# Optimization experiments

Measured on AMD Instinct MI355X. Metric: run time of the kernel, lower is better.

## Reference

```python
import jax, jax.numpy as jnp
import numpy as np

NTOKENS = 50257
NHID = 1024
NTOK_PER_CLASS = 225   # ceil(sqrt(50257))
NCLASSES = 224         # ceil(50257/225)
BATCH = 2048


def setup_inputs() -> dict:
    key = jax.random.key(0)
    k1, k2, k3, k4 = jax.random.split(key, 4)
    initrange = 0.1
    inputs = jax.random.normal(k1, (BATCH, NHID), dtype=jnp.float32)
    labels = jax.random.randint(k2, (BATCH,), 0, NTOKENS, dtype=jnp.int64)
    layer_top_W = jax.random.uniform(k3, (NHID, NCLASSES), dtype=jnp.float32,
                                     minval=-initrange, maxval=initrange)
    layer_top_b = jnp.zeros((NCLASSES,), dtype=jnp.float32)
    layer_bottom_W = jax.random.uniform(k4, (NCLASSES, NHID, NTOK_PER_CLASS),
                                        dtype=jnp.float32,
                                        minval=-initrange, maxval=initrange)
    layer_bottom_b = jnp.zeros((NCLASSES, NTOK_PER_CLASS), dtype=jnp.float32)
    return {"inputs": inputs, "labels": labels,
            "layer_top_W": layer_top_W, "layer_top_b": layer_top_b,
            "layer_bottom_W": layer_bottom_W, "layer_bottom_b": layer_bottom_b}


def reference(inputs, labels, layer_top_W, layer_top_b, layer_bottom_W, layer_bottom_b):
    batch_size = inputs.shape[0]
    label_position_top = labels // NTOK_PER_CLASS          # [B]
    label_position_bottom = labels % NTOK_PER_CLASS        # [B]

    # top-level class probabilities
    top_logits = inputs @ layer_top_W + layer_top_b        # [B, nclasses]
    top_probs = jax.nn.softmax(top_logits, axis=1)

    # per-sample gather of class weight matrices + batched matmul
    W_sel = layer_bottom_W[label_position_top]             # [B, nhid, ntok_per_class]
    b_sel = layer_bottom_b[label_position_top]             # [B, ntok_per_class]
    bottom_logits = jnp.einsum('bh,bht->bt', inputs, W_sel) + b_sel
    bottom_probs = jax.nn.softmax(bottom_logits, axis=1)

    idx = jnp.arange(batch_size)
    target_probs = top_probs[idx, label_position_top] * bottom_probs[idx, label_position_bottom]
    return target_probs
```

## Files before the change

kernel.cpp:

```cpp
#include <hip/hip_runtime.h>
#include <math.h>

#define NHID  1024
#define NCLS  224
#define NTPC  225
#define BATCH 2048

#define KSPLIT 8
#define KCH    128
#define NTILES (BATCH / 16)
#define NBOT_BLOCKS (NCLS * KSPLIT)
#define NTOP_BLOCKS (NTILES * KSPLIT)

#define YTS 224
#define YBS 228
#define YTOPK (BATCH * YTS)
#define YBOTK (BATCH * YBS)

#define CLS_OFF  0
#define POS_OFF  8192
#define LIST_OFF 16384
#define OFFS_OFF 24576
#define YTOP_OFF 32768
#define YTOP_BYTES (KSPLIT * YTOPK * 4)
#define YBOT_OFF (YTOP_OFF + YTOP_BYTES)
#define YBOT_BYTES (KSPLIT * YBOTK * 4)

typedef float f4u __attribute__((ext_vector_type(4), aligned(4)));

__global__ __launch_bounds__(256) void group_kernel(const int* __restrict__ labels,
                                                    int* __restrict__ cls,
                                                    int* __restrict__ pos,
                                                    int* __restrict__ list,
                                                    int* __restrict__ offs) {
    __shared__ int cnt[NCLS];
    __shared__ int sc[256];
    __shared__ int bex[NCLS];
    __shared__ int nz;
    const int tid = threadIdx.x;
    if (tid == 0) nz = 0;
    for (int j = tid; j < NCLS; j += 256) cnt[j] = 0;
    __syncthreads();
    int loc = 0;
    for (int k = 0; k < 4; ++k) {
        int i = tid + 256 * k;
        if (labels[2 * i + 1] != 0) loc = 1;
    }
    if (loc) atomicOr(&nz, 1);
    __syncthreads();
    const bool is64 = (nz == 0);
    int myc[8], myr[8];
#pragma unroll
    for (int k = 0; k < 8; ++k) {
        int i = tid + 256 * k;
        int l = is64 ? labels[2 * i] : labels[i];
        int c = l / NTPC;
        cls[i] = c;
        pos[i] = l - c * NTPC;
        myc[k] = c;
        myr[k] = atomicAdd(&cnt[c], 1);
    }
    __syncthreads();
    int v = (tid < NCLS) ? cnt[tid] : 0;
    sc[tid] = v;
    __syncthreads();
    for (int off = 1; off < 256; off <<= 1) {
        int u = (tid >= off) ? sc[tid - off] : 0;
        __syncthreads();
        sc[tid] += u;
        __syncthreads();
    }
    if (tid < NCLS) {
        int ex = sc[tid] - v;
        bex[tid] = ex;
        offs[tid] = ex;
    }
    if (tid == 0) offs[NCLS] = BATCH;
    __syncthreads();
#pragma unroll
    for (int k = 0; k < 8; ++k) {
        int i = tid + 256 * k;
        list[bex[myc[k]] + myr[k]] = i;
    }
}

template<int YC, int YS, bool BOT>
__device__ __forceinline__ void run_tiles(const float* __restrict__ x,
                                          const float* __restrict__ W,
                                          float* __restrict__ yk,
                                          const int* __restrict__ list,
                                          int o, int n, int hbase,
                                          float* __restrict__ xs) {
    const int tid = threadIdx.x;
    const int w = tid >> 6, l = tid & 63;
    const int cb  = 4 * l;
    const int cbc = min(cb, YC - 4);
    const int r  = tid & 127;
    const int hs = tid >> 7;
    const int rq = (r >> 1) & 3;
    const float4* xsq = (const float4*)xs;

    for (int tile = 0; tile * 16 < n; ++tile) {
        if (tile) __syncthreads();
        const float* xrow = x + hbase + r;
#pragma unroll
        for (int j = 0; j < 8; ++j) {
            const int i = hs * 8 + j;
            const int idx = tile * 16 + i;
            const int s = BOT ? list[o + min(idx, n - 1)] : (o + idx);
            xs[(r << 4) + ((((i >> 2) ^ rq) << 2) | (i & 3))] = xrow[(size_t)s * NHID];
        }
        __syncthreads();

        float4 acc[4];
#pragma unroll
        for (int i = 0; i < 4; ++i) acc[i] = make_float4(0.f, 0.f, 0.f, 0.f);

        auto compute4 = [&](int hb, int ph, const f4u (&wv)[4]) {
#pragma unroll
            for (int j = 0; j < 4; ++j) {
                const float4 xv = xsq[(hb + j) * 4 + (w ^ (ph + (j >> 1)))];
                const f4u wq = wv[j];
                acc[0].x = fmaf(xv.x, wq.x, acc[0].x);
                acc[0].y = fmaf(xv.x, wq.y, acc[0].y);
                acc[0].z = fmaf(xv.x, wq.z, acc[0].z);
                acc[0].w = fmaf(xv.x, wq.w, acc[0].w);
                acc[1].x = fmaf(xv.y, wq.x, acc[1].x);
                acc[1].y = fmaf(xv.y, wq.y, acc[1].y);
                acc[1].z = fmaf(xv.y, wq.z, acc[1].z);
                acc[1].w = fmaf(xv.y, wq.w, acc[1].w);
                acc[2].x = fmaf(xv.z, wq.x, acc[2].x);
                acc[2].y = fmaf(xv.z, wq.y, acc[2].y);
                acc[2].z = fmaf(xv.z, wq.z, acc[2].z);
                acc[2].w = fmaf(xv.z, wq.w, acc[2].w);
                acc[3].x = fmaf(xv.w, wq.x, acc[3].x);
                acc[3].y = fmaf(xv.w, wq.y, acc[3].y);
                acc[3].z = fmaf(xv.w, wq.z, acc[3].z);
                acc[3].w = fmaf(xv.w, wq.w, acc[3].w);
            }
        };

        const float* wp = W + (size_t)hbase * YC + cbc;
        f4u wva[4], wvb[4];
#pragma unroll
        for (int j = 0; j < 4; ++j)
            wva[j] = *(const f4u*)(wp + (size_t)j * YC);

#pragma unroll 1
        for (int h0 = 0; h0 < KCH; h0 += 8) {
            const float* wpb = wp + 4 * (size_t)YC;
#pragma unroll
            for (int j = 0; j < 4; ++j)
                wvb[j] = *(const f4u*)(wpb + (size_t)j * YC);
            compute4(h0, 0, wva);
            const float* wpa = wp + ((h0 + 8 < KCH) ? 8 : 0) * (size_t)YC;
#pragma unroll
            for (int j = 0; j < 4; ++j)
                wva[j] = *(const f4u*)(wpa + (size_t)j * YC);
            compute4(h0 + 4, 2, wvb);
            wp += 8 * (size_t)YC;
        }

        const int nt = min(n - tile * 16, 16);
#pragma unroll
        for (int jj = 0; jj < 4; ++jj) {
            const int it = 4 * w + jj;
            if (it < nt) {
                const int s = BOT ? list[o + tile * 16 + it] : (o + tile * 16 + it);
                float* yr = yk + (size_t)s * YS;
                if (cb + 3 < YC) {
                    *(float4*)(yr + cb) = acc[jj];
                } else if (cb < YC) {
                    yr[cb] = acc[jj].w;
                }
            }
        }
    }
}

__global__ __launch_bounds__(256, 4) void partial_kernel(const float* __restrict__ x,
                                                         const float* __restrict__ Wt,
                                                         const float* __restrict__ Wb,
                                                         const int* __restrict__ list,
                                                         const int* __restrict__ offs,
                                                         float* __restrict__ ytop,
                                                         float* __restrict__ ybot) {
    __shared__ __align__(16) float xs[KCH * 16];
    const int bi = blockIdx.x;
    if (bi < NBOT_BLOCKS) {
        const int c = bi % NCLS;
        const int k = bi / NCLS;
        const int o = offs[c];
        const int n = offs[c + 1] - o;
        run_tiles<NTPC, YBS, true>(x, Wb + (size_t)c * (NHID * NTPC),
                                   ybot + (size_t)k * YBOTK, list, o, n, k * KCH, xs);
    } else {
        const int b2 = bi - NBOT_BLOCKS;
        const int st = b2 % NTILES;
        const int k  = b2 / NTILES;
        run_tiles<NCLS, YTS, false>(x, Wt, ytop + (size_t)k * YTOPK, list,
                                    st * 16, 16, k * KCH, xs);
    }
}

__global__ __launch_bounds__(256) void finalize_kernel(const float* __restrict__ ytop,
                                                       const float* __restrict__ ybot,
                                                       const float* __restrict__ bt,
                                                       const float* __restrict__ bb,
                                                       const int* __restrict__ cls,
                                                       const int* __restrict__ pos,
                                                       float* __restrict__ out) {
    const int w = threadIdx.x >> 6, l = threadIdx.x & 63;
    const int s = blockIdx.x * 4 + w;
    const int c = cls[s], p = pos[s];

    float v[4];
#pragma unroll
    for (int g = 0; g < 4; ++g) {
        int col = l + 64 * g;
        if (col < NCLS) {
            float a = bt[col];
#pragma unroll
            for (int k = 0; k < KSPLIT; ++k)
                a += ytop[(size_t)k * YTOPK + (size_t)s * YTS + col];
            v[g] = a;
        } else {
            v[g] = -INFINITY;
        }
    }
    float mx = fmaxf(fmaxf(v[0], v[1]), fmaxf(v[2], v[3]));
#pragma unroll
    for (int off = 32; off; off >>= 1) mx = fmaxf(mx, __shfl_xor(mx, off));
    float sum = 0.f, tc = 0.f;
#pragma unroll
    for (int g = 0; g < 4; ++g) {
        int col = l + 64 * g;
        float e = (col < NCLS) ? __expf(v[g] - mx) : 0.f;
        sum += e;
        if (col == c) tc = e;
    }
#pragma unroll
    for (int off = 32; off; off >>= 1) {
        sum += __shfl_xor(sum, off);
        tc  += __shfl_xor(tc, off);
    }
    const float tp = tc / sum;

#pragma unroll
    for (int g = 0; g < 4; ++g) {
        int col = l + 64 * g;
        if (col < NTPC) {
            float a = bb[c * NTPC + col];
#pragma unroll
            for (int k = 0; k < KSPLIT; ++k)
                a += ybot[(size_t)k * YBOTK + (size_t)s * YBS + col];
            v[g] = a;
        } else {
            v[g] = -INFINITY;
        }
    }
    mx = fmaxf(fmaxf(v[0], v[1]), fmaxf(v[2], v[3]));
#pragma unroll
    for (int off = 32; off; off >>= 1) mx = fmaxf(mx, __shfl_xor(mx, off));
    float bsum = 0.f, ep = 0.f;
#pragma unroll
    for (int g = 0; g < 4; ++g) {
        int col = l + 64 * g;
        float e = (col < NTPC) ? __expf(v[g] - mx) : 0.f;
        bsum += e;
        if (col == p) ep = e;
    }
#pragma unroll
    for (int off = 32; off; off >>= 1) bsum += __shfl_xor(bsum, off);
#pragma unroll
    for (int g = 0; g < 4; ++g)
        if (l + 64 * g == p) out[s] = tp * ep / bsum;
}

extern "C" void kernel_launch(void* const* d_in, const int* in_sizes, int n_in,
                              void* d_out, int out_size, void* d_ws, size_t ws_size,
                              hipStream_t stream) {
    const float* inputs = (const float*)d_in[0];
    const int*   labels = (const int*)d_in[1];
    const float* topW   = (const float*)d_in[2];
    const float* topB   = (const float*)d_in[3];
    const float* botW   = (const float*)d_in[4];
    const float* botB   = (const float*)d_in[5];
    float* out = (float*)d_out;

    char* ws   = (char*)d_ws;
    int*   cls = (int*)(ws + CLS_OFF);
    int*   pos = (int*)(ws + POS_OFF);
    int*   lst = (int*)(ws + LIST_OFF);
    int*   off = (int*)(ws + OFFS_OFF);
    float* ytop = (float*)(ws + YTOP_OFF);
    float* ybot = (float*)(ws + YBOT_OFF);

    group_kernel<<<1, 256, 0, stream>>>(labels, cls, pos, lst, off);
    partial_kernel<<<NBOT_BLOCKS + NTOP_BLOCKS, 256, 0, stream>>>(
        inputs, topW, botW, lst, off, ytop, ybot);
    finalize_kernel<<<BATCH / 4, 256, 0, stream>>>(ytop, ybot, topB, botB, cls, pos, out);
}
```

Baseline: 333.8 us.

## Stage weight tiles into LDS via async global_load_lds with a producer wave

Weight rows are no longer read straight from global memory into registers. One dedicated wave issues asynchronous global-to-LDS DMA copies into a double-buffered LDS slot, synchronised with manual waitcnt and barriers, so weight fetches overlap compute. Each block now processes two 16-sample tiles per pass over the weights, halving weight traffic per sample. The LDS footprint grows, so occupancy drops from 4 to 3 blocks per SIMD launch bound. This adds padding and tail-fix logic for unaligned 225-wide rows, which carries a correctness risk.

```diff
diff --git a/kernel.cpp b/kernel.cpp
--- a/kernel.cpp
+++ b/kernel.cpp
@@ -16,6 +16,11 @@
 #define YBS 228
 #define YTOPK (BATCH * YTS)
 #define YBOTK (BATCH * YBS)
+
+#define RPAD 228
+#define WSLOT (16 * RPAD)
+#define XS_OFF (2 * WSLOT)
+#define LDS_FLOATS (2 * WSLOT + 2 * 2048)
 
 #define CLS_OFF  0
 #define POS_OFF  8192
@@ -26,7 +31,36 @@
 #define YBOT_OFF (YTOP_OFF + YTOP_BYTES)
 #define YBOT_BYTES (KSPLIT * YBOTK * 4)
 
-typedef float f4u __attribute__((ext_vector_type(4), aligned(4)));
+#define SBAR() __builtin_amdgcn_s_barrier()
+#define LGKM0() do { asm volatile("s_waitcnt lgkmcnt(0)" ::: "memory"); \
+                     __builtin_amdgcn_sched_barrier(0); } while (0)
+#define VM15() do { asm volatile("s_waitcnt vmcnt(15)" ::: "memory"); \
+                    __builtin_amdgcn_sched_barrier(0); } while (0)
+#define VM0()  do { asm volatile("s_waitcnt vmcnt(0)" ::: "memory"); \
+                    __builtin_amdgcn_sched_barrier(0); } while (0)
+
+__device__ __forceinline__ void dma16(const float* src, float* dst) {
+    __builtin_amdgcn_global_load_lds(
+        (const __attribute__((address_space(1))) void*)src,
+        (__attribute__((address_space(3))) void*)dst, 16, 0, 0);
+}
+
+template<int RBF>
+__device__ __forceinline__ void issue_group(const float* chunk, const float* wend,
+                                            float* wslot, int g, int l) {
+    const float* gb = chunk + (size_t)g * 16 * RBF;
+#pragma unroll
+    for (int i = 0; i < 15; ++i) {
+        if (i < 14 || l < 16) {
+            const int c = 64 * i + l;
+            const int row = c / 57;
+            const int b = c - row * 57;
+            const float* src = gb + row * RBF + b * 4;
+            if (src + 4 > wend) src = wend - 4;
+            dma16(src, wslot + i * 256);
+        }
+    }
+}
 
 __global__ __launch_bounds__(256) void group_kernel(const int* __restrict__ labels,
                                                     int* __restrict__ cls,
@@ -84,122 +118,143 @@
     }
 }
 
-template<int YC, int YS, bool BOT>
+template<int YC, int YS, int RBF, bool BOT>
 __device__ __forceinline__ void run_tiles(const float* __restrict__ x,
-                                          const float* __restrict__ W,
+                                          const float* __restrict__ chunk,
+                                          const float* __restrict__ wend,
                                           float* __restrict__ yk,
                                           const int* __restrict__ list,
                                           int o, int n, int hbase,
-                                          float* __restrict__ xs) {
+                                          float* __restrict__ lds) {
+    float* wlds = lds;
+    float* xsb  = lds + XS_OFF;
     const int tid = threadIdx.x;
     const int w = tid >> 6, l = tid & 63;
-    const int cb  = 4 * l;
-    const int cbc = min(cb, YC - 4);
+    const bool pw = (w == 3);
     const int r  = tid & 127;
     const int hs = tid >> 7;
     const int rq = (r >> 1) & 3;
-    const float4* xsq = (const float4*)xs;
-
-    for (int tile = 0; tile * 16 < n; ++tile) {
-        if (tile) __syncthreads();
-        const float* xrow = x + hbase + r;
-#pragma unroll
-        for (int j = 0; j < 8; ++j) {
-            const int i = hs * 8 + j;
-            const int idx = tile * 16 + i;
-            const int s = BOT ? list[o + min(idx, n - 1)] : (o + idx);
-            xs[(r << 4) + ((((i >> 2) ^ rq) << 2) | (i & 3))] = xrow[(size_t)s * NHID];
-        }
-        __syncthreads();
-
-        float4 acc[4];
-#pragma unroll
-        for (int i = 0; i < 4; ++i) acc[i] = make_float4(0.f, 0.f, 0.f, 0.f);
-
-        auto compute4 = [&](int hb, int ph, const f4u (&wv)[4]) {
-#pragma unroll
-            for (int j = 0; j < 4; ++j) {
-                const float4 xv = xsq[(hb + j) * 4 + (w ^ (ph + (j >> 1)))];
-                const f4u wq = wv[j];
-                acc[0].x = fmaf(xv.x, wq.x, acc[0].x);
-                acc[0].y = fmaf(xv.x, wq.y, acc[0].y);
-                acc[0].z = fmaf(xv.x, wq.z, acc[0].z);
-                acc[0].w = fmaf(xv.x, wq.w, acc[0].w);
-                acc[1].x = fmaf(xv.y, wq.x, acc[1].x);
-                acc[1].y = fmaf(xv.y, wq.y, acc[1].y);
-                acc[1].z = fmaf(xv.y, wq.z, acc[1].z);
-                acc[1].w = fmaf(xv.y, wq.w, acc[1].w);
-                acc[2].x = fmaf(xv.z, wq.x, acc[2].x);
-                acc[2].y = fmaf(xv.z, wq.y, acc[2].y);
-                acc[2].z = fmaf(xv.z, wq.z, acc[2].z);
-                acc[2].w = fmaf(xv.z, wq.w, acc[2].w);
-                acc[3].x = fmaf(xv.w, wq.x, acc[3].x);
-                acc[3].y = fmaf(xv.w, wq.y, acc[3].y);
-                acc[3].z = fmaf(xv.w, wq.z, acc[3].z);
-                acc[3].w = fmaf(xv.w, wq.w, acc[3].w);
-            }
-        };
-
-        const float* wp = W + (size_t)hbase * YC + cbc;
-        f4u wva[4], wvb[4];
-#pragma unroll
-        for (int j = 0; j < 4; ++j)
-            wva[j] = *(const f4u*)(wp + (size_t)j * YC);
-
-#pragma unroll 1
-        for (int h0 = 0; h0 < KCH; h0 += 8) {
-            const float* wpb = wp + 4 * (size_t)YC;
-#pragma unroll
-            for (int j = 0; j < 4; ++j)
-                wvb[j] = *(const f4u*)(wpb + (size_t)j * YC);
-            compute4(h0, 0, wva);
-            const float* wpa = wp + ((h0 + 8 < KCH) ? 8 : 0) * (size_t)YC;
-#pragma unroll
-            for (int j = 0; j < 4; ++j)
-                wva[j] = *(const f4u*)(wpa + (size_t)j * YC);
-            compute4(h0 + 4, 2, wvb);
-            wp += 8 * (size_t)YC;
-        }
-
-        const int nt = min(n - tile * 16, 16);
-#pragma unroll
-        for (int jj = 0; jj < 4; ++jj) {
-            const int it = 4 * w + jj;
-            if (it < nt) {
-                const int s = BOT ? list[o + tile * 16 + it] : (o + tile * 16 + it);
-                float* yr = yk + (size_t)s * YS;
-                if (cb + 3 < YC) {
-                    *(float4*)(yr + cb) = acc[jj];
-                } else if (cb < YC) {
-                    yr[cb] = acc[jj].w;
+    const int lq = min(4 * l, RPAD - 4);
+    const bool fixtail = BOT && (chunk + 128 * RBF == wend);
+
+    for (int sb = 0; sb < n; sb += 32) {
+        const int nb = min(n - sb, 32);
+        const int ntile = (nb + 15) >> 4;
+
+#pragma unroll
+        for (int t = 0; t < 2; ++t) if (t < ntile) {
+            int sid[8];
+#pragma unroll
+            for (int j = 0; j < 8; ++j) {
+                const int idx = sb + t * 16 + hs * 8 + j;
+                sid[j] = BOT ? list[o + min(idx, n - 1)] : (o + min(idx, n - 1));
+            }
+            const float* xr = x + hbase + r;
+            float* xst = xsb + t * 2048;
+#pragma unroll
+            for (int j = 0; j < 8; ++j) {
+                const int i = hs * 8 + j;
+                xst[(r << 4) + ((((i >> 2) ^ rq) << 2) | (i & 3))] =
+                    xr[(size_t)sid[j] * NHID];
+            }
+        }
+        LGKM0();
+        if (pw) {
+            issue_group<RBF>(chunk, wend, wlds, 0, l);
+            issue_group<RBF>(chunk, wend, wlds + WSLOT, 1, l);
+        }
+
+        float4 acc[2][4];
+#pragma unroll
+        for (int t = 0; t < 2; ++t)
+#pragma unroll
+            for (int s = 0; s < 4; ++s) acc[t][s] = make_float4(0.f, 0.f, 0.f, 0.f);
+
+        for (int g = 0; g < 8; ++g) {
+            if (pw) {
+                if (g == 7) { VM0(); } else { VM15(); }
+                if (fixtail && g == 7) {
+                    if (l == 0)
+                        wlds[WSLOT + 15 * RPAD + 224] = wend[-1];
+                    LGKM0();
                 }
             }
-        }
-    }
-}
-
-__global__ __launch_bounds__(256, 4) void partial_kernel(const float* __restrict__ x,
+            SBAR();
+            const float* wl = wlds + (g & 1) * WSLOT;
+#pragma unroll
+            for (int t = 0; t < 2; ++t) if (t < ntile) {
+                const float4* xq = (const float4*)(xsb + t * 2048);
+#pragma unroll
+                for (int j = 0; j < 16; ++j) {
+                    const float4 wv = *(const float4*)(wl + j * RPAD + lq);
+                    const float4 xv = xq[(g * 16 + j) * 4 + (w ^ ((j >> 1) & 3))];
+                    acc[t][0].x = fmaf(xv.x, wv.x, acc[t][0].x);
+                    acc[t][0].y = fmaf(xv.x, wv.y, acc[t][0].y);
+                    acc[t][0].z = fmaf(xv.x, wv.z, acc[t][0].z);
+                    acc[t][0].w = fmaf(xv.x, wv.w, acc[t][0].w);
+                    acc[t][1].x = fmaf(xv.y, wv.x, acc[t][1].x);
+                    acc[t][1].y = fmaf(xv.y, wv.y, acc[t][1].y);
+                    acc[t][1].z = fmaf(xv.y, wv.z, acc[t][1].z);
+                    acc[t][1].w = fmaf(xv.y, wv.w, acc[t][1].w);
+                    acc[t][2].x = fmaf(xv.z, wv.x, acc[t][2].x);
+                    acc[t][2].y = fmaf(xv.z, wv.y, acc[t][2].y);
+                    acc[t][2].z = fmaf(xv.z, wv.z, acc[t][2].z);
+                    acc[t][2].w = fmaf(xv.z, wv.w, acc[t][2].w);
+                    acc[t][3].x = fmaf(xv.w, wv.x, acc[t][3].x);
+                    acc[t][3].y = fmaf(xv.w, wv.y, acc[t][3].y);
+                    acc[t][3].z = fmaf(xv.w, wv.z, acc[t][3].z);
+                    acc[t][3].w = fmaf(xv.w, wv.w, acc[t][3].w);
+                }
+            }
+            LGKM0();
+            SBAR();
+            if (pw && g + 2 < 8)
+                issue_group<RBF>(chunk, wend, wlds + (g & 1) * WSLOT, g + 2, l);
+        }
+
+        const int cb = 4 * l;
+#pragma unroll
+        for (int t = 0; t < 2; ++t) if (t < ntile) {
+#pragma unroll
+            for (int jj = 0; jj < 4; ++jj) {
+                const int it = 4 * w + jj;
+                if (t * 16 + it < nb && cb < YC) {
+                    const int gi = o + sb + t * 16 + it;
+                    const int s = BOT ? list[gi] : gi;
+                    *(float4*)(yk + (size_t)s * YS + cb) = acc[t][jj];
+                }
+            }
+        }
+    }
+}
+
+__global__ __launch_bounds__(256, 3) void partial_kernel(const float* __restrict__ x,
                                                          const float* __restrict__ Wt,
                                                          const float* __restrict__ Wb,
                                                          const int* __restrict__ list,
                                                          const int* __restrict__ offs,
                                                          float* __restrict__ ytop,
                                                          float* __restrict__ ybot) {
-    __shared__ __align__(16) float xs[KCH * 16];
+    __shared__ __align__(16) float lds[LDS_FLOATS];
     const int bi = blockIdx.x;
     if (bi < NBOT_BLOCKS) {
         const int c = bi % NCLS;
         const int k = bi / NCLS;
         const int o = offs[c];
         const int n = offs[c + 1] - o;
-        run_tiles<NTPC, YBS, true>(x, Wb + (size_t)c * (NHID * NTPC),
-                                   ybot + (size_t)k * YBOTK, list, o, n, k * KCH, xs);
+        if (n == 0) return;
+        const float* chunk = Wb + (size_t)c * (NHID * NTPC) + (size_t)(k * KCH) * NTPC;
+        const float* wend  = Wb + (size_t)NCLS * NHID * NTPC;
+        run_tiles<NTPC, YBS, NTPC, true>(x, chunk, wend, ybot + (size_t)k * YBOTK,
+                                         list, o, n, k * KCH, lds);
     } else {
         const int b2 = bi - NBOT_BLOCKS;
         const int st = b2 % NTILES;
         const int k  = b2 / NTILES;
-        run_tiles<NCLS, YTS, false>(x, Wt, ytop + (size_t)k * YTOPK, list,
-                                    st * 16, 16, k * KCH, xs);
+        const float* chunk = Wt + (size_t)(k * KCH) * NCLS;
+        const float* wend  = Wt + (size_t)NHID * NCLS;
+        run_tiles<NCLS, YTS, NCLS, false>(x, chunk, wend, ytop + (size_t)k * YTOPK,
+                                          list, st * 16, 16, k * KCH, lds);
     }
 }
 
```

New measurement: 652.4 us. +95.5%, slower.
